# Kernel tuning notes

Hardware: AMD Instinct MI355X
Metric: run time of the kernel (lower is better)

## Reference

```python
import jax, jax.numpy as jnp
import numpy as np

N = 50000
E = 800000
IN_DIM = 128
HEADS = 8
OUT_DIM = 32
NEG_SLOPE = 0.2


def setup_inputs() -> dict:
    key = jax.random.key(0)
    k1, k2, k3, k4, k5 = jax.random.split(key, 5)
    x = jax.random.normal(k1, (N, IN_DIM), dtype=jnp.float32)
    edge_index = jax.random.randint(k2, (2, E), 0, N, dtype=jnp.int64)
    batch = jnp.zeros((N,), dtype=jnp.int64)
    # GATConv params: glorot-style scale
    W = jax.random.normal(k3, (IN_DIM, HEADS * OUT_DIM), dtype=jnp.float32) * (1.0 / np.sqrt(IN_DIM))
    att_src = jax.random.normal(k4, (HEADS, OUT_DIM), dtype=jnp.float32) * (1.0 / np.sqrt(OUT_DIM))
    att_dst = jax.random.normal(k5, (HEADS, OUT_DIM), dtype=jnp.float32) * (1.0 / np.sqrt(OUT_DIM))
    bias = jnp.zeros((OUT_DIM,), dtype=jnp.float32)
    return {"x": x, "edge_index": edge_index, "batch": batch,
            "W": W, "att_src": att_src, "att_dst": att_dst, "bias": bias}


def reference(x, edge_index, batch, W, att_src, att_dst, bias):
    n = x.shape[0]
    h = (x @ W).reshape(n, HEADS, OUT_DIM)            # [N, H, C]
    a_src = jnp.einsum('nhc,hc->nh', h, att_src)       # [N, H]
    a_dst = jnp.einsum('nhc,hc->nh', h, att_dst)       # [N, H]
    # add self-loops (PyG default add_self_loops=True)
    loops = jnp.arange(n, dtype=edge_index.dtype)
    src = jnp.concatenate([edge_index[0], loops])
    dst = jnp.concatenate([edge_index[1], loops])
    e = jax.nn.leaky_relu(a_src[src] + a_dst[dst], NEG_SLOPE)  # [E+N, H]
    # scatter-softmax over incoming edges of each dst node
    m = jax.ops.segment_max(e, dst, num_segments=n)    # [N, H]
    m = jax.lax.stop_gradient(m)
    ex = jnp.exp(e - m[dst])
    denom = jax.ops.segment_sum(ex, dst, num_segments=n)
    alpha = ex / denom[dst]                            # [E+N, H]
    msg = h[src] * alpha[..., None]                    # [E+N, H, C]
    out = jax.ops.segment_sum(msg, dst, num_segments=n)  # [N, H, C]
    out = out.mean(axis=1) + bias                      # concat=False -> head mean
    return out
```

## Files before the change

### kernel.cpp

```cpp
#include <hip/hip_runtime.h>
#include <hip/hip_bf16.h>

#define IN_DIM 128
#define HC 256
#define HEADS 8
#define OUT_DIM 32
#define NEG_SLOPE 0.2f
#define ELL_CAP 64

typedef unsigned short ushort_t;
typedef unsigned int uint_t;
typedef __attribute__((ext_vector_type(8))) short bf16x8;
typedef __attribute__((ext_vector_type(8))) unsigned short ushort8_t;
typedef __attribute__((ext_vector_type(4))) float floatx4;

__device__ inline ushort_t f2bf(float f) {
    uint_t u = __float_as_uint(f);
    u = (u + 0x7FFF + ((u >> 16) & 1)) >> 16;
    return (ushort_t)u;
}
__device__ inline float bf2f(ushort_t u) {
    return __uint_as_float(((uint_t)u) << 16);
}
__device__ inline uint_t pkbf(float a, float b) {
    __hip_bfloat162 t = __float22bfloat162_rn(make_float2(a, b));
    union { __hip_bfloat162 h; uint_t u; } c;
    c.h = t;
    return c.u;
}

__global__ __launch_bounds__(256) void prep_build(const float* __restrict__ W,
                                                  ushort_t* __restrict__ Wf,
                                                  const int* __restrict__ esrc,
                                                  const int* __restrict__ edst,
                                                  int* __restrict__ deg,
                                                  ushort_t* __restrict__ ell, int E) {
    const int bid = blockIdx.x;
    const int tid = threadIdx.x;
    if (bid < 16) {
        int t = bid * 256 + tid;
        int lane = t & 63;
        int ks = (t >> 6) & 3;
        int nt = t >> 8;
        int n = nt * 16 + (lane & 15);
        int k0 = ks * 32 + (lane >> 4) * 8;
        float v[8];
#pragma unroll
        for (int j = 0; j < 8; j++) v[j] = W[(size_t)(k0 + j) * HC + n];
        uint4 pk;
        pk.x = pkbf(v[0], v[1]);
        pk.y = pkbf(v[2], v[3]);
        pk.z = pkbf(v[4], v[5]);
        pk.w = pkbf(v[6], v[7]);
        *(uint4*)&Wf[(size_t)t * 8] = pk;
        return;
    }
    int i = (bid - 16) * 256 + tid;
    int base = i * 4;
    if (base + 3 < E) {
        int4 d = *(const int4*)&edst[base];
        int4 s = *(const int4*)&esrc[base];
        int r0 = atomicAdd(&deg[d.x], 1);
        int r1 = atomicAdd(&deg[d.y], 1);
        int r2 = atomicAdd(&deg[d.z], 1);
        int r3 = atomicAdd(&deg[d.w], 1);
        if (r0 < ELL_CAP) ell[d.x * ELL_CAP + r0] = (ushort_t)s.x;
        if (r1 < ELL_CAP) ell[d.y * ELL_CAP + r1] = (ushort_t)s.y;
        if (r2 < ELL_CAP) ell[d.z * ELL_CAP + r2] = (ushort_t)s.z;
        if (r3 < ELL_CAP) ell[d.w * ELL_CAP + r3] = (ushort_t)s.w;
    } else {
        for (int j = base; j < E; j++) {
            int r = atomicAdd(&deg[edst[j]], 1);
            if (r < ELL_CAP) ell[edst[j] * ELL_CAP + r] = (ushort_t)esrc[j];
        }
    }
}

__global__ __launch_bounds__(256) void gemm_mfma(const float* __restrict__ x,
                                                 const ushort_t* __restrict__ Wf,
                                                 const float* __restrict__ att_s,
                                                 const float* __restrict__ att_d,
                                                 ushort_t* __restrict__ h2,
                                                 float* __restrict__ a_src,
                                                 float* __restrict__ a_dst, int N) {
    __shared__ ushort_t xs[128 * 136];
    const int tid = threadIdx.x;
    const int row0 = blockIdx.x * 128;
#pragma unroll
    for (int i = 0; i < 16; i++) {
        int slot = tid + i * 256;
        int r = slot >> 5, kq = slot & 31;
        int gr = row0 + r;
        float4 v = (gr < N) ? *(const float4*)&x[(size_t)gr * IN_DIM + kq * 4]
                            : make_float4(0.f, 0.f, 0.f, 0.f);
        uint2 pk;
        pk.x = pkbf(v.x, v.y);
        pk.y = pkbf(v.z, v.w);
        *(uint2*)&xs[r * 136 + kq * 4] = pk;
    }
    __syncthreads();

    const int lane = tid & 63;
    const int w = tid >> 6;
    const int wm = (w & 1) * 64;
    const int colblk = blockIdx.y * 128 + (w >> 1) * 64;
    const int m15 = lane & 15, quad = lane >> 4;

    floatx4 acc[4][4] = {};
#pragma unroll
    for (int ks = 0; ks < 4; ks++) {
        bf16x8 a[4], b[4];
#pragma unroll
        for (int mt = 0; mt < 4; mt++)
            a[mt] = *(const bf16x8*)&xs[(wm + mt * 16 + m15) * 136 + ks * 32 + quad * 8];
#pragma unroll
        for (int nt = 0; nt < 4; nt++) {
            int ntg = (colblk >> 4) + nt;
            b[nt] = *(const bf16x8*)&Wf[(size_t)(((ntg * 4 + ks) * 64) + lane) * 8];
        }
#pragma unroll
        for (int mt = 0; mt < 4; mt++)
#pragma unroll
            for (int nt = 0; nt < 4; nt++)
                acc[mt][nt] = __builtin_amdgcn_mfma_f32_16x16x32_bf16(a[mt], b[nt], acc[mt][nt], 0, 0, 0);
    }

    const int cbase = colblk + m15;
    const int head0 = colblk >> 5;
    float as0 = att_s[colblk + m15],      as1 = att_s[colblk + 16 + m15];
    float as2 = att_s[colblk + 32 + m15], as3 = att_s[colblk + 48 + m15];
    float ad0 = att_d[colblk + m15],      ad1 = att_d[colblk + 16 + m15];
    float ad2 = att_d[colblk + 32 + m15], ad3 = att_d[colblk + 48 + m15];
#pragma unroll
    for (int mt = 0; mt < 4; mt++) {
#pragma unroll
        for (int reg = 0; reg < 4; reg++) {
            int gr = row0 + wm + mt * 16 + quad * 4 + reg;
            float sA = acc[mt][0][reg] * as0 + acc[mt][1][reg] * as1;
            float sB = acc[mt][2][reg] * as2 + acc[mt][3][reg] * as3;
            float dA = acc[mt][0][reg] * ad0 + acc[mt][1][reg] * ad1;
            float dB = acc[mt][2][reg] * ad2 + acc[mt][3][reg] * ad3;
#pragma unroll
            for (int off = 1; off < 16; off <<= 1) {
                sA += __shfl_xor(sA, off, 64);
                sB += __shfl_xor(sB, off, 64);
                dA += __shfl_xor(dA, off, 64);
                dB += __shfl_xor(dB, off, 64);
            }
            if (gr < N) {
#pragma unroll
                for (int nt = 0; nt < 4; nt++)
                    h2[(size_t)gr * HC + cbase + nt * 16] = f2bf(acc[mt][nt][reg]);
                if (m15 == 0) {
                    a_src[gr * HEADS + head0] = sA;
                    a_src[gr * HEADS + head0 + 1] = sB;
                    a_dst[gr * HEADS + head0] = dA;
                    a_dst[gr * HEADS + head0 + 1] = dB;
                }
            }
        }
    }
}

__global__ __launch_bounds__(256) void aggregate(const ushort_t* __restrict__ h2,
                                                 const float* __restrict__ a_src,
                                                 const float* __restrict__ a_dst,
                                                 const int* __restrict__ deg,
                                                 const ushort_t* __restrict__ ell,
                                                 const float* __restrict__ bias,
                                                 float* __restrict__ out, int N) {
    int wave = threadIdx.x >> 6;
    int lane = threadIdx.x & 63;
    int n = blockIdx.x * 4 + wave;
    if (n >= N) return;
    int half = lane >> 5;
    int sl = lane & 31;
    int head = sl >> 2;
    int rowoff = sl * 8;

    float adst = a_dst[n * HEADS + head];
    float e = a_src[n * HEADS + head] + adst;
    e = fmaxf(e, NEG_SLOPE * e);
    float p = (half == 0) ? __expf(e) : 0.f;
    ushort8_t hv = *(const ushort8_t*)&h2[(size_t)n * HC + rowoff];
    float acc[8];
#pragma unroll
    for (int j = 0; j < 8; j++) acc[j] = p * bf2f(hv[j]);
    float l = p;

    int dn = __builtin_amdgcn_readfirstlane(deg[n]);
    if (dn > ELL_CAP) dn = ELL_CAP;
    const ushort_t* row = &ell[(size_t)n * ELL_CAP];
    int k = 0;
    for (; k + 7 < dn; k += 8) {
        int sidx[4];
        float ev[4];
        ushort8_t g[4];
#pragma unroll
        for (int j = 0; j < 4; j++) sidx[j] = (int)row[k + 2 * j + half];
#pragma unroll
        for (int j = 0; j < 4; j++) {
            g[j] = *(const ushort8_t*)&h2[(size_t)sidx[j] * HC + rowoff];
            ev[j] = a_src[sidx[j] * HEADS + head];
        }
#pragma unroll
        for (int j = 0; j < 4; j++) {
            float ej = ev[j] + adst;
            ej = fmaxf(ej, NEG_SLOPE * ej);
            float pj = __expf(ej);
#pragma unroll
            for (int c = 0; c < 8; c++) acc[c] += pj * bf2f(g[j][c]);
            l += pj;
        }
    }
    for (; k + 1 < dn; k += 2) {
        int s0 = (int)row[k + half];
        float e0 = a_src[s0 * HEADS + head] + adst;
        ushort8_t g0 = *(const ushort8_t*)&h2[(size_t)s0 * HC + rowoff];
        e0 = fmaxf(e0, NEG_SLOPE * e0);
        float p0 = __expf(e0);
#pragma unroll
        for (int c = 0; c < 8; c++) acc[c] += p0 * bf2f(g0[c]);
        l += p0;
    }
    if (k < dn) {
        int s0 = (int)row[k];
        float e0 = a_src[s0 * HEADS + head] + adst;
        ushort8_t g0 = *(const ushort8_t*)&h2[(size_t)s0 * HC + rowoff];
        e0 = fmaxf(e0, NEG_SLOPE * e0);
        float p0 = (half == 0) ? __expf(e0) : 0.f;
#pragma unroll
        for (int c = 0; c < 8; c++) acc[c] += p0 * bf2f(g0[c]);
        l += p0;
    }

#pragma unroll
    for (int j = 0; j < 8; j++) acc[j] += __shfl_xor(acc[j], 32, 64);
    l += __shfl_xor(l, 32, 64);

    float inv = 0.125f / l;
#pragma unroll
    for (int j = 0; j < 8; j++) acc[j] *= inv;
#pragma unroll
    for (int off = 4; off < 32; off <<= 1)
#pragma unroll
        for (int j = 0; j < 8; j++) acc[j] += __shfl_xor(acc[j], off, 64);

    if (lane < 4) {
        int c8 = sl * 8;
        float4 b0 = *(const float4*)&bias[c8];
        float4 b1 = *(const float4*)&bias[c8 + 4];
        float4 o0 = make_float4(acc[0] + b0.x, acc[1] + b0.y, acc[2] + b0.z, acc[3] + b0.w);
        float4 o1 = make_float4(acc[4] + b1.x, acc[5] + b1.y, acc[6] + b1.z, acc[7] + b1.w);
        *(float4*)&out[(size_t)n * OUT_DIM + c8] = o0;
        *(float4*)&out[(size_t)n * OUT_DIM + c8 + 4] = o1;
    }
}

extern "C" void kernel_launch(void* const* d_in, const int* in_sizes, int n_in,
                              void* d_out, int out_size, void* d_ws, size_t ws_size,
                              hipStream_t stream) {
    const float* x       = (const float*)d_in[0];
    const int*   eidx    = (const int*)d_in[1];
    const float* W       = (const float*)d_in[3];
    const float* att_src = (const float*)d_in[4];
    const float* att_dst = (const float*)d_in[5];
    const float* bias    = (const float*)d_in[6];
    float* out = (float*)d_out;

    const int N = in_sizes[0] / IN_DIM;
    const int E = in_sizes[1] / 2;
    const int* esrc = eidx;
    const int* edst = eidx + E;

    char* wsb = (char*)d_ws;
    size_t off = 0;
    auto alloc = [&](size_t bytes) -> void* {
        void* p = wsb + off;
        off = (off + bytes + 255) & ~(size_t)255;
        return p;
    };
    ushort_t* h2   = (ushort_t*)alloc((size_t)N * HC * 2);
    ushort_t* Wf   = (ushort_t*)alloc((size_t)IN_DIM * HC * 2);
    float*    a_src= (float*)alloc((size_t)N * HEADS * 4);
    float*    a_dst= (float*)alloc((size_t)N * HEADS * 4);
    int*      deg  = (int*)alloc((size_t)N * 4);
    ushort_t* ell  = (ushort_t*)alloc((size_t)N * ELL_CAP * 2);

    const int edge_blocks = (E / 4 + 255) / 256;

    hipMemsetAsync(deg, 0, (size_t)N * 4, stream);
    hipLaunchKernelGGL(prep_build, dim3(16 + edge_blocks), dim3(256), 0, stream,
                       W, Wf, esrc, edst, deg, ell, E);
    hipLaunchKernelGGL(gemm_mfma, dim3((N + 127) / 128, 2), dim3(256), 0, stream,
                       x, Wf, att_src, att_dst, h2, a_src, a_dst, N);
    hipLaunchKernelGGL(aggregate, dim3((N + 3) / 4), dim3(256), 0, stream,
                       h2, a_src, a_dst, deg, ell, bias, out, N);
}
```

Measured before the change: 219.9 us.

## Compute all 256 GEMM columns per block and transpose MFMA operands for packed stores

The GEMM grid drops its column dimension, so each block loops over two 128-column chunks and reuses the staged bf16 x tile instead of converting it twice in separate blocks. The MFMA operands are swapped (W as A, x as B) so each lane holds four consecutive columns of one row. This allows 8-byte packed bf16 stores of h in place of scattered 2-byte stores, and the attention-score reduction needs only two cross-lane shuffles. In exchange there are half as many blocks and each one does twice the work, which may lower occupancy and parallelism for the GEMM stage.

```diff
diff --git a/kernel.cpp b/kernel.cpp
--- a/kernel.cpp
+++ b/kernel.cpp
@@ -102,61 +102,71 @@
 
     const int lane = tid & 63;
     const int w = tid >> 6;
-    const int wm = (w & 1) * 64;
-    const int colblk = blockIdx.y * 128 + (w >> 1) * 64;
+    const int wrow = (w & 1) * 64;
+    const int wcol = (w >> 1) * 64;
     const int m15 = lane & 15, quad = lane >> 4;
 
-    floatx4 acc[4][4] = {};
-#pragma unroll
-    for (int ks = 0; ks < 4; ks++) {
-        bf16x8 a[4], b[4];
-#pragma unroll
-        for (int mt = 0; mt < 4; mt++)
-            a[mt] = *(const bf16x8*)&xs[(wm + mt * 16 + m15) * 136 + ks * 32 + quad * 8];
-#pragma unroll
-        for (int nt = 0; nt < 4; nt++) {
-            int ntg = (colblk >> 4) + nt;
-            b[nt] = *(const bf16x8*)&Wf[(size_t)(((ntg * 4 + ks) * 64) + lane) * 8];
-        }
-#pragma unroll
-        for (int mt = 0; mt < 4; mt++)
-#pragma unroll
-            for (int nt = 0; nt < 4; nt++)
-                acc[mt][nt] = __builtin_amdgcn_mfma_f32_16x16x32_bf16(a[mt], b[nt], acc[mt][nt], 0, 0, 0);
-    }
-
-    const int cbase = colblk + m15;
-    const int head0 = colblk >> 5;
-    float as0 = att_s[colblk + m15],      as1 = att_s[colblk + 16 + m15];
-    float as2 = att_s[colblk + 32 + m15], as3 = att_s[colblk + 48 + m15];
-    float ad0 = att_d[colblk + m15],      ad1 = att_d[colblk + 16 + m15];
-    float ad2 = att_d[colblk + 32 + m15], ad3 = att_d[colblk + 48 + m15];
-#pragma unroll
-    for (int mt = 0; mt < 4; mt++) {
-#pragma unroll
-        for (int reg = 0; reg < 4; reg++) {
-            int gr = row0 + wm + mt * 16 + quad * 4 + reg;
-            float sA = acc[mt][0][reg] * as0 + acc[mt][1][reg] * as1;
-            float sB = acc[mt][2][reg] * as2 + acc[mt][3][reg] * as3;
-            float dA = acc[mt][0][reg] * ad0 + acc[mt][1][reg] * ad1;
-            float dB = acc[mt][2][reg] * ad2 + acc[mt][3][reg] * ad3;
-#pragma unroll
-            for (int off = 1; off < 16; off <<= 1) {
-                sA += __shfl_xor(sA, off, 64);
-                sB += __shfl_xor(sB, off, 64);
-                dA += __shfl_xor(dA, off, 64);
-                dB += __shfl_xor(dB, off, 64);
-            }
-            if (gr < N) {
-#pragma unroll
-                for (int nt = 0; nt < 4; nt++)
-                    h2[(size_t)gr * HC + cbase + nt * 16] = f2bf(acc[mt][nt][reg]);
-                if (m15 == 0) {
-                    a_src[gr * HEADS + head0] = sA;
-                    a_src[gr * HEADS + head0 + 1] = sB;
-                    a_dst[gr * HEADS + head0] = dA;
-                    a_dst[gr * HEADS + head0 + 1] = dB;
+#pragma unroll
+    for (int ch = 0; ch < 2; ch++) {
+        const int colblk = wcol + ch * 128;
+        floatx4 acc[4][4] = {};
+#pragma unroll
+        for (int ks = 0; ks < 4; ks++) {
+            bf16x8 xb[4], wa[4];
+#pragma unroll
+            for (int rt = 0; rt < 4; rt++)
+                xb[rt] = *(const bf16x8*)&xs[(wrow + rt * 16 + m15) * 136 + ks * 32 + quad * 8];
+#pragma unroll
+            for (int ct = 0; ct < 4; ct++) {
+                int mtg = (colblk >> 4) + ct;
+                wa[ct] = *(const bf16x8*)&Wf[(size_t)(((mtg * 4 + ks) * 64) + lane) * 8];
+            }
+#pragma unroll
+            for (int ct = 0; ct < 4; ct++)
+#pragma unroll
+                for (int rt = 0; rt < 4; rt++)
+                    acc[ct][rt] = __builtin_amdgcn_mfma_f32_16x16x32_bf16(wa[ct], xb[rt], acc[ct][rt], 0, 0, 0);
+        }
+
+        const int hb = colblk >> 5;
+        float asc[4][4], adc[4][4];
+#pragma unroll
+        for (int ct = 0; ct < 4; ct++)
+#pragma unroll
+            for (int reg = 0; reg < 4; reg++) {
+                asc[ct][reg] = att_s[colblk + ct * 16 + quad * 4 + reg];
+                adc[ct][reg] = att_d[colblk + ct * 16 + quad * 4 + reg];
+            }
+#pragma unroll
+        for (int rt = 0; rt < 4; rt++) {
+            int gr = row0 + wrow + rt * 16 + m15;
+            bool ok = (gr < N);
+            if (ok) {
+#pragma unroll
+                for (int ct = 0; ct < 4; ct++) {
+                    uint2 pk;
+                    pk.x = pkbf(acc[ct][rt][0], acc[ct][rt][1]);
+                    pk.y = pkbf(acc[ct][rt][2], acc[ct][rt][3]);
+                    *(uint2*)&h2[(size_t)gr * HC + colblk + ct * 16 + quad * 4] = pk;
                 }
+            }
+            float sA = 0.f, sB = 0.f, dA = 0.f, dB = 0.f;
+#pragma unroll
+            for (int reg = 0; reg < 4; reg++) {
+                sA += acc[0][rt][reg] * asc[0][reg] + acc[1][rt][reg] * asc[1][reg];
+                sB += acc[2][rt][reg] * asc[2][reg] + acc[3][rt][reg] * asc[3][reg];
+                dA += acc[0][rt][reg] * adc[0][reg] + acc[1][rt][reg] * adc[1][reg];
+                dB += acc[2][rt][reg] * adc[2][reg] + acc[3][rt][reg] * adc[3][reg];
+            }
+            sA += __shfl_xor(sA, 16, 64); sA += __shfl_xor(sA, 32, 64);
+            sB += __shfl_xor(sB, 16, 64); sB += __shfl_xor(sB, 32, 64);
+            dA += __shfl_xor(dA, 16, 64); dA += __shfl_xor(dA, 32, 64);
+            dB += __shfl_xor(dB, 16, 64); dB += __shfl_xor(dB, 32, 64);
+            if (ok && quad == 0) {
+                a_src[gr * HEADS + hb]     = sA;
+                a_src[gr * HEADS + hb + 1] = sB;
+                a_dst[gr * HEADS + hb]     = dA;
+                a_dst[gr * HEADS + hb + 1] = dB;
             }
         }
     }
@@ -292,7 +302,7 @@
     hipMemsetAsync(deg, 0, (size_t)N * 4, stream);
     hipLaunchKernelGGL(prep_build, dim3(16 + edge_blocks), dim3(256), 0, stream,
                        W, Wf, esrc, edst, deg, ell, E);
-    hipLaunchKernelGGL(gemm_mfma, dim3((N + 127) / 128, 2), dim3(256), 0, stream,
+    hipLaunchKernelGGL(gemm_mfma, dim3((N + 127) / 128), dim3(256), 0, stream,
                        x, Wf, att_src, att_dst, h2, a_src, a_dst, N);
     hipLaunchKernelGGL(aggregate, dim3((N + 3) / 4), dim3(256), 0, stream,
                        h2, a_src, a_dst, deg, ell, bias, out, N);
```

Result: faster. 210.5 us (-4.3%).
